# Performance work log

Hardware: AMD Instinct MI355X
Metric: run time of the kernel (lower is better)

The kernel has to match this reference:

```python
import jax, jax.numpy as jnp
import numpy as np

B, S, K, F = 256, 512, 32, 64
H1, H2 = 512, 256


def setup_inputs() -> dict:
    key = jax.random.key(0)
    ks = jax.random.split(key, 8)
    x = jax.random.normal(ks[0], (B, S, F), dtype=jnp.float32)
    neighborhood = jax.random.randint(ks[1], (S, K), 0, S)
    distances = jax.random.uniform(ks[2], (S, K), dtype=jnp.float32)
    in_w = K * (F + 1)  # 2080
    W1 = jax.random.normal(ks[3], (in_w, H1), dtype=jnp.float32) * 0.02
    b1 = jnp.zeros((H1,), dtype=jnp.float32)
    W2 = jax.random.normal(ks[4], (H1, H2), dtype=jnp.float32) * 0.02
    b2 = jnp.zeros((H2,), dtype=jnp.float32)
    Wd = jax.random.normal(ks[5], (H2, 1), dtype=jnp.float32) * 0.02
    bd = jnp.zeros((1,), dtype=jnp.float32)
    return {"x": x, "neighborhood": neighborhood, "distances": distances,
            "W1": W1, "b1": b1, "W2": W2, "b2": b2, "Wd": Wd, "bd": bd}


def reference(x, neighborhood, distances, W1, b1, W2, b2, Wd, bd):
    b, s, f = x.shape
    k = neighborhood.shape[1]
    # make_k_tensor: gather neighbors and append per-edge distance
    gathered = x[:, neighborhood, :]                      # [B, S, K, F]
    dist = jnp.broadcast_to(distances[None, :, :, None], (b, s, k, 1))
    kt = jnp.concatenate([gathered, dist], axis=-1)        # [B, S, K, F+1]
    # filter phase: shared MLP over flattened neighborhoods
    flat = kt.reshape(b * s, k * (f + 1))                  # [B*S, K*(F+1)]
    h = jax.nn.relu(flat @ W1 + b1)
    h = h @ W2 + b2                                        # [B*S, H2]
    h = h.reshape(b, s, -1)
    # max pool over sequence, then final dense
    m = jnp.max(h, axis=1)                                 # [B, H2]
    out = jax.nn.relu(m) @ Wd + bd                         # [B, 1]
    return out.squeeze(1)                                  # [B]
```

## Files before the change

kernel.cpp:

```cpp
#include <hip/hip_runtime.h>

typedef __attribute__((ext_vector_type(8))) short short8;
typedef __attribute__((ext_vector_type(4))) float f32x4;

constexpr int Bb = 256, Ss = 512, Kk = 32, Ff = 64, H1 = 512, H2 = 256;
constexpr int Mtot = Bb * Ss;
constexpr int Mh = Mtot / 2;
constexpr int KD1 = Kk * Ff;

#define DEVI static __device__ __forceinline__
#define BARRIER asm volatile("s_barrier" ::: "memory")
#define VMCNT(N) asm volatile("s_waitcnt vmcnt(" #N ")" ::: "memory")

DEVI unsigned short f2b(float f) {
  unsigned u = __float_as_uint(f);
  return (unsigned short)((u + 0x7FFFu + ((u >> 16) & 1u)) >> 16);
}

DEVI void stage16(const void* g, void* l) {
  __builtin_amdgcn_global_load_lds((const __attribute__((address_space(1))) void*)g,
                                   (__attribute__((address_space(3))) void*)l, 16, 0, 0);
}

__global__ void k_cvt_x(const float* __restrict__ x, unsigned short* __restrict__ xbf) {
  int i = blockIdx.x * 256 + threadIdx.x;
  float4 v = ((const float4*)x)[i];
  ushort4 o;
  o.x = f2b(v.x); o.y = f2b(v.y); o.z = f2b(v.z); o.w = f2b(v.w);
  ((ushort4*)xbf)[i] = o;
}

__global__ void k_w1t(const float* __restrict__ W1, unsigned short* __restrict__ w1t) {
  int idx = blockIdx.x * 256 + threadIdx.x;
  int h = idx >> 11, i = idx & 2047;
  int k = i >> 6, f = i & 63;
  w1t[idx] = f2b(W1[(k * 65 + f) * 512 + h]);
}

__global__ void k_w2t(const float* __restrict__ W2, unsigned short* __restrict__ w2t) {
  int idx = blockIdx.x * 256 + threadIdx.x;
  int n = idx >> 9, k = idx & 511;
  w2t[idx] = f2b(W2[k * 256 + n]);
}

__global__ void k_dbias(const float* __restrict__ W1, const float* __restrict__ b1,
                        const float* __restrict__ dist, float* __restrict__ dbias) {
  int idx = blockIdx.x * 256 + threadIdx.x;
  int s = idx >> 9, h = idx & 511;
  float a = b1[h];
  #pragma unroll
  for (int k = 0; k < 32; ++k)
    a += dist[s * 32 + k] * W1[(k * 65 + 64) * 512 + h];
  dbias[idx] = a;
}


__global__ __launch_bounds__(512, 2) void k_gemm1(
    const unsigned short* __restrict__ xbf, const unsigned short* __restrict__ w1t,
    const int* __restrict__ nb, const float* __restrict__ dbias,
    unsigned short* __restrict__ h1, int mbase) {
  __shared__ __align__(16) unsigned short lds[2][2][256 * 64];
  const int tid = threadIdx.x;
  const int lane = tid & 63;
  const int w = tid >> 6;
  const int wm = w >> 2, wn = w & 3;
  const int mblk = blockIdx.x >> 1;
  const int nblk = blockIdx.x & 1;
  const int r0l = mblk << 8;
  const int r0g = mbase + r0l;
  const int b = r0g >> 9;
  const int s0 = r0g & 511;
  const int ncol0 = nblk << 8;
  const int scol8 = (((lane & 7) ^ ((lane >> 3) & 7)) << 3);

  int nbi[4];
  #pragma unroll
  for (int u = 0; u < 4; ++u)
    nbi[u] = (s0 + (u << 6) + (w << 3) + (lane >> 3)) << 5;

  f32x4 acc[8][4];
  #pragma unroll
  for (int m = 0; m < 8; ++m)
    #pragma unroll
    for (int n = 0; n < 4; ++n) acc[m][n] = (f32x4){0.f, 0.f, 0.f, 0.f};

  #pragma unroll
  for (int u = 0; u < 4; ++u) {
    int j = nb[nbi[u]];
    stage16(xbf + (((size_t)((b << 9) + j)) << 6) + scol8,
            &lds[0][0][(u << 12) + (w << 9)]);
  }
  #pragma unroll
  for (int u = 0; u < 4; ++u)
    stage16(w1t + (((size_t)(ncol0 + (u << 6) + (w << 3) + (lane >> 3))) << 11) + scol8,
            &lds[0][1][(u << 12) + (w << 9)]);
  int j4[4];
  #pragma unroll
  for (int u = 0; u < 4; ++u) j4[u] = nb[nbi[u] + 1];
  VMCNT(0);
  BARRIER;

  for (int t = 0; t < 32; ++t) {
    unsigned short* As = &lds[t & 1][0][0];
    unsigned short* Bs = &lds[t & 1][1][0];
    unsigned short* An = &lds[(t & 1) ^ 1][0][0];
    unsigned short* Bn = &lds[(t & 1) ^ 1][1][0];
    const bool pf = (t < 31);
    short8 a[4], bq[4];
    int jn[4];

#define RD_A(mq, ks)                                                             \
    _Pragma("unroll")                                                            \
    for (int i = 0; i < 4; ++i)                                                  \
      a[i] = *(const short8*)(As + ((wm << 7) + ((mq) << 6) + (i << 4) +         \
               (lane & 15)) * 64 + (((((ks) << 2) + (lane >> 4)) ^ (lane & 7)) << 3));
#define RD_B(ks)                                                                 \
    _Pragma("unroll")                                                            \
    for (int n = 0; n < 4; ++n)                                                  \
      bq[n] = *(const short8*)(Bs + ((wn << 6) + (n << 4) + (lane & 15)) * 64 +  \
               (((((ks) << 2) + (lane >> 4)) ^ (lane & 7)) << 3));
#define STA(u) stage16(xbf + (((size_t)((b << 9) + j4[u])) << 6) + scol8,        \
                       An + ((u) << 12) + (w << 9))
#define STB(u) stage16(w1t + (((size_t)(ncol0 + ((u) << 6) + (w << 3) +          \
                       (lane >> 3))) << 11) + ((t + 1) << 6) + scol8,            \
                       Bn + ((u) << 12) + (w << 9))
#define MM(mq)                                                                   \
    _Pragma("unroll")                                                            \
    for (int i = 0; i < 4; ++i)                                                  \
      _Pragma("unroll")                                                          \
      for (int n = 0; n < 4; ++n)                                                \
        acc[((mq) << 2) + i][n] = __builtin_amdgcn_mfma_f32_16x16x32_bf16(       \
            a[i], bq[n], acc[((mq) << 2) + i][n], 0, 0, 0);

    RD_A(0, 0); RD_B(0);
    if (pf) { STA(0); STA(2); VMCNT(2); } else { VMCNT(0); }
    BARRIER;
    __builtin_amdgcn_s_setprio(1); MM(0); __builtin_amdgcn_s_setprio(0);
    BARRIER;
    RD_A(1, 0);
    if (pf) { STB(0); STB(1); }
    BARRIER;
    __builtin_amdgcn_s_setprio(1); MM(1); __builtin_amdgcn_s_setprio(0);
    BARRIER;
    RD_A(0, 1); RD_B(1);
    {
      int tt = (t + 2 < 32) ? (t + 2) : 31;
      #pragma unroll
      for (int u = 0; u < 4; ++u) jn[u] = nb[nbi[u] + tt];
    }
    if (pf) { STB(2); STB(3); }
    BARRIER;
    __builtin_amdgcn_s_setprio(1); MM(0); __builtin_amdgcn_s_setprio(0);
    BARRIER;
    RD_A(1, 1);
    if (pf) { STA(1); STA(3); VMCNT(2); }
    BARRIER;
    __builtin_amdgcn_s_setprio(1); MM(1); __builtin_amdgcn_s_setprio(0);
    BARRIER;

    #pragma unroll
    for (int u = 0; u < 4; ++u) j4[u] = jn[u];
#undef RD_A
#undef RD_B
#undef STA
#undef STB
#undef MM
  }

  #pragma unroll
  for (int fm = 0; fm < 8; ++fm) {
    int rowl = (wm << 7) + (fm << 4) + ((lane >> 4) << 2);
    #pragma unroll
    for (int n = 0; n < 4; ++n) {
      int col = ncol0 + (wn << 6) + (n << 4) + (lane & 15);
      #pragma unroll
      for (int r = 0; r < 4; ++r) {
        int rl = rowl + r;
        float v = acc[fm][n][r] + dbias[((((r0g + rl) & 511)) << 9) + col];
        v = v > 0.f ? v : 0.f;
        h1[((size_t)(r0l + rl) << 9) + col] = f2b(v);
      }
    }
  }
}

__global__ __launch_bounds__(256, 2) void k_gemm2(
    const unsigned short* __restrict__ h1, const unsigned short* __restrict__ w2t,
    const float* __restrict__ b2, unsigned* __restrict__ mrelu, int mbase) {
  __shared__ __align__(16) unsigned short As[128 * 64];
  __shared__ __align__(16) unsigned short Bs[256 * 64];
  const int tid = threadIdx.x;
  const int lane = tid & 63;
  const int w = tid >> 6;
  const int r0l = blockIdx.x << 7;
  const int b = (mbase + r0l) >> 9;
  const int scol8 = (((lane & 7) ^ ((lane >> 3) & 7)) << 3);

  f32x4 acc[8][4];
  #pragma unroll
  for (int m = 0; m < 8; ++m)
    #pragma unroll
    for (int n = 0; n < 4; ++n) acc[m][n] = (f32x4){0.f, 0.f, 0.f, 0.f};

  for (int t = 0; t < 8; ++t) {
    #pragma unroll
    for (int a2 = 0; a2 < 4; ++a2)
      stage16(h1 + (((size_t)(r0l + (w << 5) + (a2 << 3) + (lane >> 3))) << 9) +
                  (t << 6) + scol8,
              As + (w << 11) + (a2 << 9));
    #pragma unroll
    for (int b2i = 0; b2i < 8; ++b2i)
      stage16(w2t + (((size_t)((w << 6) + (b2i << 3) + (lane >> 3))) << 9) +
                  (t << 6) + scol8,
              Bs + (w << 12) + (b2i << 9));
    VMCNT(0);
    __syncthreads();
    #pragma unroll
    for (int ks = 0; ks < 2; ++ks) {
      const int rdoff = ((((ks << 2) + (lane >> 4)) ^ (lane & 7)) << 3);
      short8 af[8], bf[4];
      #pragma unroll
      for (int fm = 0; fm < 8; ++fm)
        af[fm] = *(const short8*)(As + ((fm << 4) + (lane & 15)) * 64 + rdoff);
      #pragma unroll
      for (int n = 0; n < 4; ++n)
        bf[n] = *(const short8*)(Bs + ((w << 6) + (n << 4) + (lane & 15)) * 64 + rdoff);
      #pragma unroll
      for (int fm = 0; fm < 8; ++fm)
        #pragma unroll
        for (int n = 0; n < 4; ++n)
          acc[fm][n] = __builtin_amdgcn_mfma_f32_16x16x32_bf16(af[fm], bf[n], acc[fm][n], 0, 0, 0);
    }
    __syncthreads();
  }

  #pragma unroll
  for (int n = 0; n < 4; ++n) {
    int col = (w << 6) + (n << 4) + (lane & 15);
    float cm = -1e30f;
    #pragma unroll
    for (int fm = 0; fm < 8; ++fm)
      #pragma unroll
      for (int r = 0; r < 4; ++r) cm = fmaxf(cm, acc[fm][n][r]);
    cm = fmaxf(cm, __shfl_xor(cm, 16));
    cm = fmaxf(cm, __shfl_xor(cm, 32));
    if ((lane >> 4) == 0) {
      float v = fmaxf(cm + b2[col], 0.f);
      atomicMax(mrelu + ((b << 8) + col), __float_as_uint(v));
    }
  }
}

__global__ void k_final(const unsigned* __restrict__ mrelu, const float* __restrict__ wd,
                        const float* __restrict__ bd, float* __restrict__ out) {
  int b = blockIdx.x, t = threadIdx.x;
  float v = __uint_as_float(mrelu[(b << 8) + t]) * wd[t];
  #pragma unroll
  for (int o = 32; o > 0; o >>= 1) v += __shfl_down(v, o);
  __shared__ float p[4];
  if ((t & 63) == 0) p[t >> 6] = v;
  __syncthreads();
  if (t == 0) out[b] = p[0] + p[1] + p[2] + p[3] + bd[0];
}

extern "C" void kernel_launch(void* const* d_in, const int* in_sizes, int n_in,
                              void* d_out, int out_size, void* d_ws, size_t ws_size,
                              hipStream_t stream) {
  (void)in_sizes; (void)n_in; (void)out_size; (void)ws_size;
  const float* x    = (const float*)d_in[0];
  const int*   nb   = (const int*)d_in[1];
  const float* dist = (const float*)d_in[2];
  const float* W1   = (const float*)d_in[3];
  const float* b1   = (const float*)d_in[4];
  const float* W2   = (const float*)d_in[5];
  const float* b2   = (const float*)d_in[6];
  const float* Wd   = (const float*)d_in[7];
  const float* bd   = (const float*)d_in[8];
  float* out = (float*)d_out;

  char* p = (char*)d_ws;
  unsigned short* xbf   = (unsigned short*)p; p += (size_t)Bb * Ss * Ff * 2;
  unsigned short* w1t   = (unsigned short*)p; p += (size_t)H1 * KD1 * 2;
  unsigned short* w2t   = (unsigned short*)p; p += (size_t)H2 * H1 * 2;
  float*          dbias = (float*)p;          p += (size_t)Ss * H1 * 4;
  unsigned*       mrelu = (unsigned*)p;       p += (size_t)Bb * H2 * 4;
  unsigned short* h1    = (unsigned short*)p; p += (size_t)Mh * H1 * 2;

  hipMemsetAsync(mrelu, 0, (size_t)Bb * H2 * 4, stream);
  k_cvt_x<<<(Bb * Ss * Ff / 4) / 256, 256, 0, stream>>>(x, xbf);
  k_w1t<<<(H1 * KD1) / 256, 256, 0, stream>>>(W1, w1t);
  k_w2t<<<(H2 * H1) / 256, 256, 0, stream>>>(W2, w2t);
  k_dbias<<<(Ss * H1) / 256, 256, 0, stream>>>(W1, b1, dist, dbias);
  for (int hh = 0; hh < 2; ++hh) {
    int mbase = hh * Mh;
    k_gemm1<<<(Mh / 256) * (H1 / 256), 512, 0, stream>>>(xbf, w1t, nb, dbias, h1, mbase);
    k_gemm2<<<(Mh / 128), 256, 0, stream>>>(h1, w2t, b2, mrelu, mbase);
  }
  k_final<<<Bb, 256, 0, stream>>>(mrelu, Wd, bd, out);
}
```

Baseline: 408.7 us.

## Tile gemm1 by sequence position across batches with 4-stage K pipeline

```diff
diff --git a/kernel.cpp b/kernel.cpp
--- a/kernel.cpp
+++ b/kernel.cpp
@@ -54,29 +54,39 @@
   dbias[idx] = a;
 }
 
-
 __global__ __launch_bounds__(512, 2) void k_gemm1(
     const unsigned short* __restrict__ xbf, const unsigned short* __restrict__ w1t,
     const int* __restrict__ nb, const float* __restrict__ dbias,
-    unsigned short* __restrict__ h1, int mbase) {
-  __shared__ __align__(16) unsigned short lds[2][2][256 * 64];
+    unsigned short* __restrict__ h1, int sbase) {
+  __shared__ __align__(16) unsigned short lds[4][2][8192];
+  __shared__ int jlds[32];
   const int tid = threadIdx.x;
   const int lane = tid & 63;
   const int w = tid >> 6;
   const int wm = w >> 2, wn = w & 3;
-  const int mblk = blockIdx.x >> 1;
+  const int sblk = blockIdx.x >> 1;
+  const int s = sbase + sblk;
   const int nblk = blockIdx.x & 1;
-  const int r0l = mblk << 8;
-  const int r0g = mbase + r0l;
-  const int b = r0g >> 9;
-  const int s0 = r0g & 511;
   const int ncol0 = nblk << 8;
-  const int scol8 = (((lane & 7) ^ ((lane >> 3) & 7)) << 3);
-
-  int nbi[4];
-  #pragma unroll
-  for (int u = 0; u < 4; ++u)
-    nbi[u] = (s0 + (u << 6) + (w << 3) + (lane >> 3)) << 5;
+  const int ds = sblk;
+
+  if (tid < 32) jlds[tid] = nb[(s << 5) + tid];
+
+  const int slotb = (lane & 7) ^ (lane >> 3);
+  const int rSt = (w << 4) + ((lane >> 3) << 1) + (slotb >> 2);
+  const int cSt8 = (slotb & 3) << 3;
+  const size_t aBase0 = ((size_t)rSt << 15);
+  const size_t aBase1 = ((size_t)(rSt + 128) << 15);
+  const size_t bBase0 = ((size_t)(ncol0 + rSt) << 11);
+  const size_t bBase1 = ((size_t)(ncol0 + rSt + 128) << 11);
+  const int dstL = (w << 9) + (lane << 3);
+
+  const int r0 = lane & 15, cF = lane >> 4;
+  const int q0 = r0 >> 1;
+  const int sl0 = cF + ((r0 & 1) << 2);
+  const int sig0e = (((q0 << 3) + (sl0 ^ q0)) << 3);
+  const int sA0 = (wm << 12) + sig0e;
+  const int sB0 = (wn << 11) + sig0e;
 
   f32x4 acc[8][4];
   #pragma unroll
@@ -84,101 +94,72 @@
     #pragma unroll
     for (int n = 0; n < 4; ++n) acc[m][n] = (f32x4){0.f, 0.f, 0.f, 0.f};
 
-  #pragma unroll
-  for (int u = 0; u < 4; ++u) {
-    int j = nb[nbi[u]];
-    stage16(xbf + (((size_t)((b << 9) + j)) << 6) + scol8,
-            &lds[0][0][(u << 12) + (w << 9)]);
-  }
-  #pragma unroll
-  for (int u = 0; u < 4; ++u)
-    stage16(w1t + (((size_t)(ncol0 + (u << 6) + (w << 3) + (lane >> 3))) << 11) + scol8,
-            &lds[0][1][(u << 12) + (w << 9)]);
-  int j4[4];
-  #pragma unroll
-  for (int u = 0; u < 4; ++u) j4[u] = nb[nbi[u] + 1];
-  VMCNT(0);
-  BARRIER;
-
-  for (int t = 0; t < 32; ++t) {
-    unsigned short* As = &lds[t & 1][0][0];
-    unsigned short* Bs = &lds[t & 1][1][0];
-    unsigned short* An = &lds[(t & 1) ^ 1][0][0];
-    unsigned short* Bn = &lds[(t & 1) ^ 1][1][0];
-    const bool pf = (t < 31);
-    short8 a[4], bq[4];
-    int jn[4];
-
-#define RD_A(mq, ks)                                                             \
-    _Pragma("unroll")                                                            \
-    for (int i = 0; i < 4; ++i)                                                  \
-      a[i] = *(const short8*)(As + ((wm << 7) + ((mq) << 6) + (i << 4) +         \
-               (lane & 15)) * 64 + (((((ks) << 2) + (lane >> 4)) ^ (lane & 7)) << 3));
-#define RD_B(ks)                                                                 \
-    _Pragma("unroll")                                                            \
-    for (int n = 0; n < 4; ++n)                                                  \
-      bq[n] = *(const short8*)(Bs + ((wn << 6) + (n << 4) + (lane & 15)) * 64 +  \
-               (((((ks) << 2) + (lane >> 4)) ^ (lane & 7)) << 3));
-#define STA(u) stage16(xbf + (((size_t)((b << 9) + j4[u])) << 6) + scol8,        \
-                       An + ((u) << 12) + (w << 9))
-#define STB(u) stage16(w1t + (((size_t)(ncol0 + ((u) << 6) + (w << 3) +          \
-                       (lane >> 3))) << 11) + ((t + 1) << 6) + scol8,            \
-                       Bn + ((u) << 12) + (w << 9))
-#define MM(mq)                                                                   \
-    _Pragma("unroll")                                                            \
-    for (int i = 0; i < 4; ++i)                                                  \
-      _Pragma("unroll")                                                          \
-      for (int n = 0; n < 4; ++n)                                                \
-        acc[((mq) << 2) + i][n] = __builtin_amdgcn_mfma_f32_16x16x32_bf16(       \
-            a[i], bq[n], acc[((mq) << 2) + i][n], 0, 0, 0);
-
-    RD_A(0, 0); RD_B(0);
-    if (pf) { STA(0); STA(2); VMCNT(2); } else { VMCNT(0); }
+  __syncthreads();
+
+#define STAGE_WIN(WIN)                                                          \
+  {                                                                             \
+    const int HS = ((WIN) < 63) ? (WIN) : 63;                                   \
+    const int tS = HS >> 1, hS = HS & 1;                                        \
+    const int slS = (WIN) & 3;                                                  \
+    const int jS = jlds[tS];                                                    \
+    const size_t ko = ((size_t)hS << 5) + cSt8;                                 \
+    const size_t ja = ((size_t)jS << 6);                                        \
+    stage16(xbf + aBase0 + ja + ko, &lds[slS][0][dstL]);                        \
+    stage16(xbf + aBase1 + ja + ko, &lds[slS][0][4096 + dstL]);                 \
+    stage16(w1t + bBase0 + ((size_t)HS << 5) + cSt8, &lds[slS][1][dstL]);       \
+    stage16(w1t + bBase1 + ((size_t)HS << 5) + cSt8, &lds[slS][1][4096 + dstL]); \
+  }
+
+  STAGE_WIN(0);
+  STAGE_WIN(1);
+  STAGE_WIN(2);
+  VMCNT(8);
+
+  #pragma unroll 4
+  for (int W = 0; W < 64; ++W) {
     BARRIER;
-    __builtin_amdgcn_s_setprio(1); MM(0); __builtin_amdgcn_s_setprio(0);
-    BARRIER;
-    RD_A(1, 0);
-    if (pf) { STB(0); STB(1); }
-    BARRIER;
-    __builtin_amdgcn_s_setprio(1); MM(1); __builtin_amdgcn_s_setprio(0);
-    BARRIER;
-    RD_A(0, 1); RD_B(1);
-    {
-      int tt = (t + 2 < 32) ? (t + 2) : 31;
-      #pragma unroll
-      for (int u = 0; u < 4; ++u) jn[u] = nb[nbi[u] + tt];
-    }
-    if (pf) { STB(2); STB(3); }
-    BARRIER;
-    __builtin_amdgcn_s_setprio(1); MM(0); __builtin_amdgcn_s_setprio(0);
-    BARRIER;
-    RD_A(1, 1);
-    if (pf) { STA(1); STA(3); VMCNT(2); }
-    BARRIER;
-    __builtin_amdgcn_s_setprio(1); MM(1); __builtin_amdgcn_s_setprio(0);
-    BARRIER;
-
-    #pragma unroll
-    for (int u = 0; u < 4; ++u) j4[u] = jn[u];
-#undef RD_A
-#undef RD_B
-#undef STA
-#undef STB
-#undef MM
-  }
-
-  #pragma unroll
-  for (int fm = 0; fm < 8; ++fm) {
-    int rowl = (wm << 7) + (fm << 4) + ((lane >> 4) << 2);
-    #pragma unroll
-    for (int n = 0; n < 4; ++n) {
-      int col = ncol0 + (wn << 6) + (n << 4) + (lane & 15);
+    const int sl4 = W & 3;
+    const unsigned short* Ar = &lds[sl4][0][0];
+    const unsigned short* Br = &lds[sl4][1][0];
+    short8 a0[4], a1[4], bF[4];
+    #pragma unroll
+    for (int i = 0; i < 4; ++i) a0[i] = *(const short8*)(Ar + sA0 + (i << 9));
+    #pragma unroll
+    for (int n = 0; n < 4; ++n) bF[n] = *(const short8*)(Br + sB0 + (n << 9));
+    #pragma unroll
+    for (int i = 0; i < 4; ++i) a1[i] = *(const short8*)(Ar + sA0 + 2048 + (i << 9));
+
+    STAGE_WIN(W + 3);
+    VMCNT(8);
+
+    __builtin_amdgcn_s_setprio(1);
+    #pragma unroll
+    for (int i = 0; i < 4; ++i)
+      #pragma unroll
+      for (int n = 0; n < 4; ++n)
+        acc[i][n] = __builtin_amdgcn_mfma_f32_16x16x32_bf16(a0[i], bF[n], acc[i][n], 0, 0, 0);
+    #pragma unroll
+    for (int i = 0; i < 4; ++i)
+      #pragma unroll
+      for (int n = 0; n < 4; ++n)
+        acc[4 + i][n] = __builtin_amdgcn_mfma_f32_16x16x32_bf16(a1[i], bF[n], acc[4 + i][n], 0, 0, 0);
+    __builtin_amdgcn_s_setprio(0);
+  }
+#undef STAGE_WIN
+
+  #pragma unroll
+  for (int n = 0; n < 4; ++n) {
+    const int col = ncol0 + (wn << 6) + (n << 4) + (lane & 15);
+    const float dv = dbias[(s << 9) + col];
+    #pragma unroll
+    for (int fm = 0; fm < 8; ++fm) {
+      const int rbase = (wm << 7) + ((fm >> 2) << 6) + ((fm & 3) << 4) + ((lane >> 4) << 2);
       #pragma unroll
       for (int r = 0; r < 4; ++r) {
-        int rl = rowl + r;
-        float v = acc[fm][n][r] + dbias[((((r0g + rl) & 511)) << 9) + col];
+        const int batch = rbase + r;
+        float v = acc[fm][n][r] + dv;
         v = v > 0.f ? v : 0.f;
-        h1[((size_t)(r0l + rl) << 9) + col] = f2b(v);
+        h1[(((size_t)((batch << 8) + ds)) << 9) + col] = f2b(v);
       }
     }
   }
@@ -186,14 +167,14 @@
 
 __global__ __launch_bounds__(256, 2) void k_gemm2(
     const unsigned short* __restrict__ h1, const unsigned short* __restrict__ w2t,
-    const float* __restrict__ b2, unsigned* __restrict__ mrelu, int mbase) {
+    const float* __restrict__ b2, unsigned* __restrict__ mrelu) {
   __shared__ __align__(16) unsigned short As[128 * 64];
   __shared__ __align__(16) unsigned short Bs[256 * 64];
   const int tid = threadIdx.x;
   const int lane = tid & 63;
   const int w = tid >> 6;
   const int r0l = blockIdx.x << 7;
-  const int b = (mbase + r0l) >> 9;
+  const int b = r0l >> 8;
   const int scol8 = (((lane & 7) ^ ((lane >> 3) & 7)) << 3);
 
   f32x4 acc[8][4];
@@ -292,9 +273,8 @@
   k_w2t<<<(H2 * H1) / 256, 256, 0, stream>>>(W2, w2t);
   k_dbias<<<(Ss * H1) / 256, 256, 0, stream>>>(W1, b1, dist, dbias);
   for (int hh = 0; hh < 2; ++hh) {
-    int mbase = hh * Mh;
-    k_gemm1<<<(Mh / 256) * (H1 / 256), 512, 0, stream>>>(xbf, w1t, nb, dbias, h1, mbase);
-    k_gemm2<<<(Mh / 128), 256, 0, stream>>>(h1, w2t, b2, mrelu, mbase);
+    k_gemm1<<<512, 512, 0, stream>>>(xbf, w1t, nb, dbias, h1, hh * 256);
+    k_gemm2<<<Mh / 128, 256, 0, stream>>>(h1, w2t, b2, mrelu);
   }
   k_final<<<Bb, 256, 0, stream>>>(mrelu, Wd, bd, out);
 }
```

Result: no change. 409.1 us (+0.1%).
